# Optimization experiments

Measured on AMD Instinct MI355X. Metric: run time of the kernel, lower is better.

## Reference

```python
import jax, jax.numpy as jnp
import numpy as np

B, SIZE, OUT = 32, 2048, 2048
EPS = 1e-5

def setup_inputs() -> dict:
    key = jax.random.key(0)
    ks = jax.random.split(key, 6)
    s = SIZE ** -0.5
    return {
        "x":    jax.random.normal(ks[0], (B, SIZE), jnp.float32),
        "Wq":   jax.random.normal(ks[1], (SIZE, SIZE), jnp.float32) * s,
        "Wk":   jax.random.normal(ks[2], (SIZE, SIZE), jnp.float32) * s,
        "Wv":   jax.random.normal(ks[3], (SIZE, SIZE), jnp.float32) * s,
        "p2":   jnp.zeros((5,), jnp.float32),              # OptimActivation params (activation2)
        "Wfc2": jax.random.normal(ks[4], (OUT, SIZE), jnp.float32) * s,
        "bfc2": jnp.zeros((OUT,), jnp.float32),
        "g2":   jnp.ones((OUT,), jnp.float32),             # LayerNorm2 weight
        "b2":   jnp.zeros((OUT,), jnp.float32),            # LayerNorm2 bias
    }

def _optim_activation(x, p):
    ps = jax.nn.softmax(p)
    # swish + sine + linear branches (sigmoid/tanh branches are computed but not summed in the original)
    return jax.nn.sigmoid(x) * x * ps[0] + jnp.sin(x) * ps[1] + x * ps[2]

def _layernorm(x, g, b):
    mu = jnp.mean(x, axis=-1, keepdims=True)
    var = jnp.mean(jnp.square(x - mu), axis=-1, keepdims=True)
    return (x - mu) * jax.lax.rsqrt(var + EPS) * g + b

def reference(x, Wq, Wk, Wv, p2, Wfc2, bfc2, g2, b2):
    q = x @ Wq.T                                   # [B, S]
    k = x @ Wk.T
    v = x @ Wv.T
    bsz, s = x.shape
    att = q[:, :, None] * k[:, None, :]            # outer product  [B, S, S]
    att = jax.nn.softmax(att.reshape(bsz, s * s), axis=-1).reshape(bsz, s, s)
    valued = jnp.einsum('bij,bj->bi', att, v)      # [B, S]
    # NOTE: original's activation/fc_linear/norm result is overwritten (dead code)
    fc = _optim_activation(valued, p2)
    fc = fc @ Wfc2.T + bfc2                        # [B, OUT]
    return _layernorm(fc, g2, b2)
```

## Files before the change

### kernel.cpp

```cpp
#include <hip/hip_runtime.h>
#include <hip/hip_bf16.h>


#define S 2048
#define BATCH 32

typedef __attribute__((ext_vector_type(8))) short short8;
typedef __attribute__((ext_vector_type(4))) float f32x4;
typedef __attribute__((ext_vector_type(2))) float f32x2;

#if __has_builtin(__builtin_elementwise_fma)
__device__ __forceinline__ f32x2 pkfma(f32x2 a, f32x2 b, f32x2 c) {
  return __builtin_elementwise_fma(a, b, c);
}
#else
__device__ __forceinline__ f32x2 pkfma(f32x2 a, f32x2 b, f32x2 c) {
  f32x2 r; r.x = fmaf(a.x, b.x, c.x); r.y = fmaf(a.y, b.y, c.y); return r;
}
#endif

__device__ __forceinline__ void cvt8t(const float* __restrict__ p, short8& hi, short8& lo) {
  const float4* p4 = (const float4*)p;
  float4 a = p4[0], b = p4[1];
  float v[8] = {a.x, a.y, a.z, a.w, b.x, b.y, b.z, b.w};
#pragma unroll
  for (int t = 0; t < 8; ++t) {
    union { float f; unsigned u; } x; x.f = v[t];
    hi[t] = (short)(x.u >> 16);
    union { unsigned u; float f; } h; h.u = x.u & 0xFFFF0000u;
    union { float f; unsigned u; } l; l.f = v[t] - h.f;
    lo[t] = (short)(l.u >> 16);
  }
}

__global__ __launch_bounds__(256) void k_qkv(
    const float* __restrict__ x,
    const float* __restrict__ Wq,
    const float* __restrict__ Wk,
    const float* __restrict__ Wv,
    float* __restrict__ qkvp,
    int* __restrict__ cnt) {
  int bid  = blockIdx.x;
  int tid  = threadIdx.x;
  if (bid == 0 && tid < BATCH) cnt[tid] = 0;
  int mi   = bid >> 8;
  int kh   = (bid >> 7) & 1;
  int nblk = bid & 127;
  const float* W = (mi == 0) ? Wq : (mi == 1) ? Wk : Wv;
  float* out = qkvp + (size_t)kh * (3 * BATCH * S) + (size_t)mi * (BATCH * S);

  int wave = tid >> 6;
  int lane = tid & 63;
  int lr   = lane & 15;
  int quad = lane >> 4;

  f32x4 acc0 = {0.f, 0.f, 0.f, 0.f};
  f32x4 acc1 = {0.f, 0.f, 0.f, 0.f};
  const float* wrow = W + (size_t)(nblk * 16 + lr) * S;
  const float* xr0  = x + (size_t)lr * S;
  const float* xr1  = x + (size_t)(lr + 16) * S;
  int kbase = kh * 1024 + wave * 256 + quad * 8;

#pragma unroll 2
  for (int ks = 0; ks < 8; ++ks) {
    int k0 = kbase + ks * 32;
    short8 bhi, blo, a0h, a0l, a1h, a1l;
    cvt8t(wrow + k0, bhi, blo);
    cvt8t(xr0 + k0, a0h, a0l);
    cvt8t(xr1 + k0, a1h, a1l);
    acc0 = __builtin_amdgcn_mfma_f32_16x16x32_bf16(a0h, bhi, acc0, 0, 0, 0);
    acc0 = __builtin_amdgcn_mfma_f32_16x16x32_bf16(a0l, bhi, acc0, 0, 0, 0);
    acc0 = __builtin_amdgcn_mfma_f32_16x16x32_bf16(a0h, blo, acc0, 0, 0, 0);
    acc1 = __builtin_amdgcn_mfma_f32_16x16x32_bf16(a1h, bhi, acc1, 0, 0, 0);
    acc1 = __builtin_amdgcn_mfma_f32_16x16x32_bf16(a1l, bhi, acc1, 0, 0, 0);
    acc1 = __builtin_amdgcn_mfma_f32_16x16x32_bf16(a1h, blo, acc1, 0, 0, 0);
  }

  __shared__ float red[4][64][8];
#pragma unroll
  for (int r = 0; r < 4; ++r) {
    red[wave][lane][r]     = acc0[r];
    red[wave][lane][4 + r] = acc1[r];
  }
  __syncthreads();
  if (tid < 64) {
    int lq = tid >> 4, lc = tid & 15;
    int n = nblk * 16 + lc;
#pragma unroll
    for (int r = 0; r < 8; ++r) {
      float s = red[0][tid][r] + red[1][tid][r] + red[2][tid][r] + red[3][tid][r];
      int m = (r < 4) ? (lq * 4 + r) : (16 + lq * 4 + (r - 4));
      out[m * S + n] = s;
    }
  }
}

__global__ __launch_bounds__(512) void k_attn(
    const float* __restrict__ qkvp, float* __restrict__ Tout, float* __restrict__ Spart,
    int* __restrict__ cnt, const float* __restrict__ p2, float* __restrict__ fc) {
  int b    = blockIdx.x >> 4;
  int iblk = blockIdx.x & 15;
  const float* qA = qkvp + (size_t)b * S;
  const float* kA = qA + BATCH * S;
  const float* vA = qA + 2 * BATCH * S;
  const float* qB = qA + 3 * BATCH * S;
  const float* kB = kA + 3 * BATCH * S;
  const float* vB = vA + 3 * BATCH * S;

  __shared__ __align__(16) float2 kv[S];
  __shared__ float qsh[128];
  __shared__ float redmx[8][4];
  __shared__ f32x2 redT[512];
  __shared__ float redS[512];
  __shared__ float Msh;
  __shared__ int lastSh;
  __shared__ float Zsh;

  int tid = threadIdx.x;
  float qmx = -1e30f, qmn = 1e30f, kmx = -1e30f, kmn = 1e30f;
  for (int idx = tid; idx < S; idx += 512) {
    float kk = kA[idx] + kB[idx];
    float vv = vA[idx] + vB[idx];
    float qq = qA[idx] + qB[idx];
    kv[idx] = make_float2(kk, vv);
    if ((idx >> 7) == iblk) qsh[idx & 127] = qq;
    qmx = fmaxf(qmx, qq); qmn = fminf(qmn, qq);
    kmx = fmaxf(kmx, kk); kmn = fminf(kmn, kk);
  }
  for (int off = 32; off; off >>= 1) {
    qmx = fmaxf(qmx, __shfl_xor(qmx, off));
    qmn = fminf(qmn, __shfl_xor(qmn, off));
    kmx = fmaxf(kmx, __shfl_xor(kmx, off));
    kmn = fminf(kmn, __shfl_xor(kmn, off));
  }
  int wave = tid >> 6, lane = tid & 63;
  if (lane == 0) {
    redmx[wave][0] = qmx; redmx[wave][1] = qmn;
    redmx[wave][2] = kmx; redmx[wave][3] = kmn;
  }
  __syncthreads();
  if (tid == 0) {
    float a = redmx[0][0], bn = redmx[0][1], c = redmx[0][2], d = redmx[0][3];
    for (int w = 1; w < 8; ++w) {
      a = fmaxf(a, redmx[w][0]); bn = fminf(bn, redmx[w][1]);
      c = fmaxf(c, redmx[w][2]); d = fminf(d, redmx[w][3]);
    }
    Msh = fmaxf(fmaxf(a * c, a * d), fmaxf(bn * c, bn * d));
  }
  __syncthreads();
  float M = Msh;

  const float LOG2E = 1.4426950408889634f;
  f32x2 aa = {qsh[lane] * LOG2E, qsh[lane + 64] * LOG2E};
  float ccs = -M * LOG2E;
  f32x2 cc = {ccs, ccs};
  f32x2 Sp = {0.f, 0.f}, Sq = {0.f, 0.f};
  f32x2 Tp = {0.f, 0.f}, Tq = {0.f, 0.f};
  int j0 = wave * 256;
#pragma unroll 4
  for (int j = j0; j < j0 + 256; j += 2) {
    float4 p = *(const float4*)&kv[j];
    f32x2 kk0 = {p.x, p.x}, vv0 = {p.y, p.y};
    f32x2 kk1 = {p.z, p.z}, vv1 = {p.w, p.w};
    f32x2 a0 = pkfma(aa, kk0, cc);
    f32x2 a1 = pkfma(aa, kk1, cc);
    f32x2 e0 = {__builtin_amdgcn_exp2f(a0.x), __builtin_amdgcn_exp2f(a0.y)};
    f32x2 e1 = {__builtin_amdgcn_exp2f(a1.x), __builtin_amdgcn_exp2f(a1.y)};
    Sp += e0;
    Sq += e1;
    Tp = pkfma(e0, vv0, Tp);
    Tq = pkfma(e1, vv1, Tq);
  }
  redT[tid] = Tp + Tq;
  redS[tid] = Sp.x + Sp.y + Sq.x + Sq.y;
  __syncthreads();
  if (tid < 128) {
    int l = tid & 63, hi = tid >> 6;
    float Tf = 0.f;
#pragma unroll
    for (int w = 0; w < 8; ++w) {
      f32x2 t = redT[w * 64 + l];
      Tf += hi ? t.y : t.x;
    }
    Tout[b * S + iblk * 128 + tid] = Tf;
  }
  if (tid < 64) {
    float Sf = 0.f;
#pragma unroll
    for (int w = 0; w < 8; ++w) Sf += redS[w * 64 + tid];
    for (int off = 32; off; off >>= 1) Sf += __shfl_xor(Sf, off);
    if (tid == 0) Spart[b * 16 + iblk] = Sf;
  }

  __syncthreads();
  if (tid == 0) {
    __threadfence();
    lastSh = (atomicAdd(&cnt[b], 1) == 15) ? 1 : 0;
  }
  __syncthreads();
  if (!lastSh) return;

  if (tid == 0) {
    float z = 0.f;
#pragma unroll
    for (int t = 0; t < 16; ++t) z += atomicAdd(&Spart[b * 16 + t], 0.f);
    Zsh = z;
  }
  __syncthreads();
  float Zinv = 1.f / Zsh;

  float p[5];
  float mx = -1e30f;
#pragma unroll
  for (int t = 0; t < 5; ++t) { p[t] = p2[t]; mx = fmaxf(mx, p[t]); }
  float se = 0.f;
#pragma unroll
  for (int t = 0; t < 5; ++t) { p[t] = __builtin_amdgcn_exp2f((p[t] - mx) * LOG2E); se += p[t]; }
  float inv = 1.f / se;
  float w0 = p[0] * inv, w1 = p[1] * inv, w2 = p[2] * inv;

  for (int i = tid; i < S; i += 512) {
    float Tv = atomicAdd(&Tout[b * S + i], 0.f);
    float val = Tv * Zinv;
    float sig = __builtin_amdgcn_rcpf(1.f + __builtin_amdgcn_exp2f(-val * LOG2E));
    float sn  = __builtin_amdgcn_sinf(val * 0.15915494309189535f);
    fc[b * S + i] = sig * val * w0 + sn * w1 + val * w2;
  }
}

__global__ __launch_bounds__(256) void k_fc(
    const float* __restrict__ fc,
    const float* __restrict__ W,
    float* __restrict__ yp) {
  int bid  = blockIdx.x;
  int kq   = bid >> 7;
  int nblk = bid & 127;
  int tid  = threadIdx.x;
  int wave = tid >> 6;
  int lane = tid & 63;
  int lr   = lane & 15;
  int quad = lane >> 4;

  f32x4 acc0 = {0.f, 0.f, 0.f, 0.f};
  f32x4 acc1 = {0.f, 0.f, 0.f, 0.f};
  const float* wrow = W + (size_t)(nblk * 16 + lr) * S;
  const float* xr0  = fc + (size_t)lr * S;
  const float* xr1  = fc + (size_t)(lr + 16) * S;
  int kbase = kq * 512 + wave * 128 + quad * 8;

#pragma unroll
  for (int ks = 0; ks < 4; ++ks) {
    int k0 = kbase + ks * 32;
    short8 bhi, blo, a0h, a0l, a1h, a1l;
    cvt8t(wrow + k0, bhi, blo);
    cvt8t(xr0 + k0, a0h, a0l);
    cvt8t(xr1 + k0, a1h, a1l);
    acc0 = __builtin_amdgcn_mfma_f32_16x16x32_bf16(a0h, bhi, acc0, 0, 0, 0);
    acc0 = __builtin_amdgcn_mfma_f32_16x16x32_bf16(a0l, bhi, acc0, 0, 0, 0);
    acc0 = __builtin_amdgcn_mfma_f32_16x16x32_bf16(a0h, blo, acc0, 0, 0, 0);
    acc1 = __builtin_amdgcn_mfma_f32_16x16x32_bf16(a1h, bhi, acc1, 0, 0, 0);
    acc1 = __builtin_amdgcn_mfma_f32_16x16x32_bf16(a1l, bhi, acc1, 0, 0, 0);
    acc1 = __builtin_amdgcn_mfma_f32_16x16x32_bf16(a1h, blo, acc1, 0, 0, 0);
  }

  __shared__ float red[4][64][8];
#pragma unroll
  for (int r = 0; r < 4; ++r) {
    red[wave][lane][r]     = acc0[r];
    red[wave][lane][4 + r] = acc1[r];
  }
  __syncthreads();
  if (tid < 64) {
    int lq = tid >> 4, lc = tid & 15;
    int n = nblk * 16 + lc;
#pragma unroll
    for (int r = 0; r < 8; ++r) {
      float s = red[0][tid][r] + red[1][tid][r] + red[2][tid][r] + red[3][tid][r];
      int m = (r < 4) ? (lq * 4 + r) : (16 + lq * 4 + (r - 4));
      yp[(size_t)kq * BATCH * S + m * S + n] = s;
    }
  }
}

__global__ __launch_bounds__(256) void k_ln(
    const float* __restrict__ yp, const float* __restrict__ bias,
    const float* __restrict__ g, const float* __restrict__ bb,
    float* __restrict__ out) {
  int b = blockIdx.x;
  const float* r0 = yp + (size_t)b * S;
  const float* r1 = r0 + BATCH * S;
  const float* r2 = r1 + BATCH * S;
  const float* r3 = r2 + BATCH * S;
  float t8[8];
  float s = 0.f, s2 = 0.f;
#pragma unroll
  for (int it = 0; it < 8; ++it) {
    int i = threadIdx.x + it * 256;
    float t = (r0[i] + r1[i]) + (r2[i] + r3[i]) + bias[i];
    t8[it] = t;
    s += t; s2 += t * t;
  }
  for (int off = 32; off; off >>= 1) {
    s  += __shfl_xor(s, off);
    s2 += __shfl_xor(s2, off);
  }
  __shared__ float rs[4], rs2[4];
  __shared__ float mu_s, r_s;
  int wave = threadIdx.x >> 6, lane = threadIdx.x & 63;
  if (lane == 0) { rs[wave] = s; rs2[wave] = s2; }
  __syncthreads();
  if (threadIdx.x == 0) {
    float S1 = rs[0] + rs[1] + rs[2] + rs[3];
    float S2 = rs2[0] + rs2[1] + rs2[2] + rs2[3];
    float mu = S1 / (float)S;
    float var = S2 / (float)S - mu * mu;
    mu_s = mu;
    r_s = rsqrtf(var + 1e-5f);
  }
  __syncthreads();
  float mu = mu_s, r = r_s;
#pragma unroll
  for (int it = 0; it < 8; ++it) {
    int i = threadIdx.x + it * 256;
    out[b * S + i] = (t8[it] - mu) * r * g[i] + bb[i];
  }
}

extern "C" void kernel_launch(void* const* d_in, const int* in_sizes, int n_in,
                              void* d_out, int out_size, void* d_ws, size_t ws_size,
                              hipStream_t stream) {
  (void)in_sizes; (void)n_in; (void)out_size; (void)ws_size;
  const float* x    = (const float*)d_in[0];
  const float* Wq   = (const float*)d_in[1];
  const float* Wk   = (const float*)d_in[2];
  const float* Wv   = (const float*)d_in[3];
  const float* p2   = (const float*)d_in[4];
  const float* Wfc2 = (const float*)d_in[5];
  const float* bfc2 = (const float*)d_in[6];
  const float* g2   = (const float*)d_in[7];
  const float* b2   = (const float*)d_in[8];
  float* out = (float*)d_out;

  float* qkvp  = (float*)d_ws;
  float* T     = qkvp + 2 * 3 * BATCH * S;
  float* Spart = T + BATCH * S;
  int*   cnt   = (int*)(Spart + BATCH * 16);
  float* fc    = (float*)(cnt + BATCH);
  float* yp    = fc + BATCH * S;

  k_qkv<<<768, 256, 0, stream>>>(x, Wq, Wk, Wv, qkvp, cnt);
  k_attn<<<512, 512, 0, stream>>>(qkvp, T, Spart, cnt, p2, fc);
  k_fc<<<512, 256, 0, stream>>>(fc, Wfc2, yp);
  k_ln<<<32, 256, 0, stream>>>(yp, bfc2, g2, b2, out);
}
```

Before: 161.4 us.

## Replace last-block epilogue in attention with per-batch spin barrier and local activation

Each attention block now publishes its partial softmax denominator with a release-counter increment, then spin-waits until all 16 blocks of its batch have arrived. After that it applies the activation to its own 128 partial outputs held in registers. This removes the T workspace round trip and the serialized last-block loop over 2048 elements. The cost is a grid-wide spin dependency: all 16 blocks of a batch must be co-resident, otherwise it deadlocks. With 512 blocks of 512 threads this relies on the GPU's occupancy.

```diff
diff --git a/kernel.cpp b/kernel.cpp
--- a/kernel.cpp
+++ b/kernel.cpp
@@ -96,7 +96,7 @@
 }
 
 __global__ __launch_bounds__(512) void k_attn(
-    const float* __restrict__ qkvp, float* __restrict__ Tout, float* __restrict__ Spart,
+    const float* __restrict__ qkvp, float* __restrict__ Spart,
     int* __restrict__ cnt, const float* __restrict__ p2, float* __restrict__ fc) {
   int b    = blockIdx.x >> 4;
   int iblk = blockIdx.x & 15;
@@ -113,7 +113,6 @@
   __shared__ f32x2 redT[512];
   __shared__ float redS[512];
   __shared__ float Msh;
-  __shared__ int lastSh;
   __shared__ float Zsh;
 
   int tid = threadIdx.x;
@@ -174,57 +173,55 @@
   redT[tid] = Tp + Tq;
   redS[tid] = Sp.x + Sp.y + Sq.x + Sq.y;
   __syncthreads();
+
+  float Tf = 0.f;
   if (tid < 128) {
     int l = tid & 63, hi = tid >> 6;
-    float Tf = 0.f;
 #pragma unroll
     for (int w = 0; w < 8; ++w) {
       f32x2 t = redT[w * 64 + l];
       Tf += hi ? t.y : t.x;
     }
-    Tout[b * S + iblk * 128 + tid] = Tf;
   }
   if (tid < 64) {
     float Sf = 0.f;
 #pragma unroll
     for (int w = 0; w < 8; ++w) Sf += redS[w * 64 + tid];
     for (int off = 32; off; off >>= 1) Sf += __shfl_xor(Sf, off);
-    if (tid == 0) Spart[b * 16 + iblk] = Sf;
-  }
-
-  __syncthreads();
+    if (tid == 0) {
+      __hip_atomic_store(&Spart[b * 16 + iblk], Sf,
+                         __ATOMIC_RELAXED, __HIP_MEMORY_SCOPE_AGENT);
+      __hip_atomic_fetch_add(&cnt[b], 1, __ATOMIC_RELEASE, __HIP_MEMORY_SCOPE_AGENT);
+    }
+  }
+
   if (tid == 0) {
-    __threadfence();
-    lastSh = (atomicAdd(&cnt[b], 1) == 15) ? 1 : 0;
-  }
-  __syncthreads();
-  if (!lastSh) return;
-
-  if (tid == 0) {
+    while (__hip_atomic_load(&cnt[b], __ATOMIC_ACQUIRE, __HIP_MEMORY_SCOPE_AGENT) < 16)
+      __builtin_amdgcn_s_sleep(1);
     float z = 0.f;
 #pragma unroll
-    for (int t = 0; t < 16; ++t) z += atomicAdd(&Spart[b * 16 + t], 0.f);
+    for (int t = 0; t < 16; ++t)
+      z += __hip_atomic_load(&Spart[b * 16 + t], __ATOMIC_RELAXED,
+                             __HIP_MEMORY_SCOPE_AGENT);
     Zsh = z;
   }
   __syncthreads();
-  float Zinv = 1.f / Zsh;
-
-  float p[5];
-  float mx = -1e30f;
-#pragma unroll
-  for (int t = 0; t < 5; ++t) { p[t] = p2[t]; mx = fmaxf(mx, p[t]); }
-  float se = 0.f;
-#pragma unroll
-  for (int t = 0; t < 5; ++t) { p[t] = __builtin_amdgcn_exp2f((p[t] - mx) * LOG2E); se += p[t]; }
-  float inv = 1.f / se;
-  float w0 = p[0] * inv, w1 = p[1] * inv, w2 = p[2] * inv;
-
-  for (int i = tid; i < S; i += 512) {
-    float Tv = atomicAdd(&Tout[b * S + i], 0.f);
-    float val = Tv * Zinv;
+
+  if (tid < 128) {
+    float Zinv = __builtin_amdgcn_rcpf(Zsh);
+    float p[5];
+    float mx = -1e30f;
+#pragma unroll
+    for (int t = 0; t < 5; ++t) { p[t] = p2[t]; mx = fmaxf(mx, p[t]); }
+    float se = 0.f;
+#pragma unroll
+    for (int t = 0; t < 5; ++t) { p[t] = __builtin_amdgcn_exp2f((p[t] - mx) * LOG2E); se += p[t]; }
+    float inv = 1.f / se;
+    float val = Tf * Zinv;
     float sig = __builtin_amdgcn_rcpf(1.f + __builtin_amdgcn_exp2f(-val * LOG2E));
     float sn  = __builtin_amdgcn_sinf(val * 0.15915494309189535f);
-    fc[b * S + i] = sig * val * w0 + sn * w1 + val * w2;
+    fc[b * S + iblk * 128 + tid] =
+        sig * val * (p[0] * inv) + sn * (p[1] * inv) + val * (p[2] * inv);
   }
 }
 
@@ -342,14 +339,13 @@
   float* out = (float*)d_out;
 
   float* qkvp  = (float*)d_ws;
-  float* T     = qkvp + 2 * 3 * BATCH * S;
-  float* Spart = T + BATCH * S;
+  float* Spart = qkvp + 2 * 3 * BATCH * S;
   int*   cnt   = (int*)(Spart + BATCH * 16);
   float* fc    = (float*)(cnt + BATCH);
   float* yp    = fc + BATCH * S;
 
   k_qkv<<<768, 256, 0, stream>>>(x, Wq, Wk, Wv, qkvp, cnt);
-  k_attn<<<512, 512, 0, stream>>>(qkvp, T, Spart, cnt, p2, fc);
+  k_attn<<<512, 512, 0, stream>>>(qkvp, Spart, cnt, p2, fc);
   k_fc<<<512, 256, 0, stream>>>(fc, Wfc2, yp);
   k_ln<<<32, 256, 0, stream>>>(yp, bfc2, g2, b2, out);
 }
```

New measurement: 163.7 us. Within noise of the previous version (+1.4%).
